# Performance work log

Hardware: AMD Instinct MI355X
Metric: run time of the kernel (lower is better)

## Reference

```python
import jax, jax.numpy as jnp
import numpy as np

N, F, H, FO = 4096, 512, 4, 128  # nodes, in-feat, heads, out-feat per head
NEG_INF = -1e10
LRELU_ALPHA = 0.2


def setup_inputs() -> dict:
    key = jax.random.key(0)
    k_x, k_a, k_w, k_as, k_an = jax.random.split(key, 5)
    X = jax.random.normal(k_x, (N, F), dtype=jnp.float32)
    A = (jax.random.uniform(k_a, (N, N)) < 0.01).astype(jnp.float32)
    A = jnp.minimum(A + jnp.eye(N, dtype=jnp.float32), 1.0)
    W = jax.random.normal(k_w, (H, F, FO), dtype=jnp.float32) * 0.05       # per-head kernels
    b = jnp.zeros((H, FO), dtype=jnp.float32)                               # per-head biases
    a_self = jax.random.normal(k_as, (H, FO), dtype=jnp.float32) * 0.05    # attn_kernel_self (F_,1) per head
    a_neigh = jax.random.normal(k_an, (H, FO), dtype=jnp.float32) * 0.05   # attn_kernel_neigh (F_,1) per head
    return {"X": X, "A": A, "W": W, "b": b, "a_self": a_self, "a_neigh": a_neigh}


def reference(X, A, W, b, a_self, a_neigh):
    # features[h] = X @ W[h] -> [H, N, FO]
    feats = jnp.einsum('nf,hfo->hno', X, W)
    # Nx1 self / neighbor scores per head -> [H, N]
    e_s = jnp.einsum('hno,ho->hn', feats, a_self)
    e_n = jnp.einsum('hno,ho->hn', feats, a_neigh)
    # broadcast-add to [H, N, N], LeakyReLU(0.2), additive adjacency mask
    logits = e_s[:, :, None] + e_n[:, None, :]
    logits = jnp.where(logits > 0, logits, LRELU_ALPHA * logits)
    logits = logits + NEG_INF * (1.0 - A)[None, :, :]
    attn = jax.nn.softmax(logits, axis=-1)          # [H, N, N]
    out = jnp.einsum('hnm,hmo->hno', attn, feats)   # weighted aggregate
    out = out + b[:, None, :]
    # concat heads: [N, H*FO]
    out = jnp.transpose(out, (1, 0, 2)).reshape(X.shape[0], -1)
    return jax.nn.relu(out)
```

## Files before the change

### kernel.cpp

```cpp
#include <hip/hip_runtime.h>
#include <math.h>

#define NODES 4096
#define FIN   512
#define HEADS 4
#define FOUT  128
#define COLS  512

typedef short  short8  __attribute__((ext_vector_type(8)));
typedef float  floatx4 __attribute__((ext_vector_type(4)));

__device__ inline void split8(const float4& a, const float4& b, short8& hi, short8& lo) {
    float v[8] = {a.x, a.y, a.z, a.w, b.x, b.y, b.z, b.w};
    #pragma unroll
    for (int i = 0; i < 8; i++) {
        unsigned xb = __float_as_uint(v[i]);
        unsigned hb = xb & 0xFFFF0000u;
        hi[i] = (short)(hb >> 16);
        float r = v[i] - __uint_as_float(hb);
        lo[i] = (short)(__float_as_uint(r) >> 16);
    }
}

__global__ __launch_bounds__(256) void convert_w(
    const float* __restrict__ W, short* __restrict__ Wthi, short* __restrict__ Wtlo)
{
    int t = blockIdx.x * 256 + threadIdx.x;
    int o = t & 127;
    int hs = t >> 7;
    int h = hs >> 6, seg = hs & 63;
    float4 a, b;
    float va[8];
    #pragma unroll
    for (int i = 0; i < 8; i++)
        va[i] = W[((size_t)(h * FIN) + seg * 8 + i) * FOUT + o];
    a = make_float4(va[0], va[1], va[2], va[3]);
    b = make_float4(va[4], va[5], va[6], va[7]);
    short8 hi, lo; split8(a, b, hi, lo);
    size_t dst = (size_t)(h * FOUT + o) * FIN + seg * 8;
    *(short8*)&Wthi[dst] = hi;
    *(short8*)&Wtlo[dst] = lo;
}

__global__ __launch_bounds__(256) void gemm_mfma(
    const float* __restrict__ X,
    const short* __restrict__ Bthi, const short* __restrict__ Btlo,
    float* __restrict__ feats)
{
    __shared__ short Ah[2][64][40], Al[2][64][40], Bh[2][64][40], Bl[2][64][40];
    const int tid = threadIdx.x;
    const int rowBase = blockIdx.y * 64;
    const int colBase = blockIdx.x * 64;
    const int lane = tid & 63, w = tid >> 6;
    const int quad = lane >> 4, lk = quad * 8, lm = lane & 15;
    const int sr = tid >> 2;
    const int sk = (tid & 3) * 8;

    const float* xp = X + (size_t)(rowBase + sr) * FIN + sk;
    const short* bhp = Bthi + (size_t)(colBase + sr) * FIN + sk;
    const short* blp = Btlo + (size_t)(colBase + sr) * FIN + sk;

    floatx4 acc[4];
    #pragma unroll
    for (int mi = 0; mi < 4; mi++) acc[mi] = (floatx4)0.f;

    float4 xa = *(const float4*)(xp);
    float4 xb = *(const float4*)(xp + 4);
    short8 rbh = *(const short8*)(bhp);
    short8 rbl = *(const short8*)(blp);

    for (int it = 0; it < FIN / 32; ++it) {
        const int cur = it & 1;
        short8 hi, lo; split8(xa, xb, hi, lo);
        *(short8*)&Ah[cur][sr][sk] = hi;
        *(short8*)&Al[cur][sr][sk] = lo;
        *(short8*)&Bh[cur][sr][sk] = rbh;
        *(short8*)&Bl[cur][sr][sk] = rbl;
        if (it + 1 < FIN / 32) {
            int k0 = (it + 1) * 32;
            xa  = *(const float4*)(xp + k0);
            xb  = *(const float4*)(xp + k0 + 4);
            rbh = *(const short8*)(bhp + k0);
            rbl = *(const short8*)(blp + k0);
        }
        __syncthreads();

        short8 afh[4], afl[4];
        #pragma unroll
        for (int mi = 0; mi < 4; mi++) {
            afh[mi] = *(const short8*)&Ah[cur][mi * 16 + lm][lk];
            afl[mi] = *(const short8*)&Al[cur][mi * 16 + lm][lk];
        }
        short8 bfh = *(const short8*)&Bh[cur][w * 16 + lm][lk];
        short8 bfl = *(const short8*)&Bl[cur][w * 16 + lm][lk];
        #pragma unroll
        for (int mi = 0; mi < 4; mi++) {
            acc[mi] = __builtin_amdgcn_mfma_f32_16x16x32_bf16(afh[mi], bfh, acc[mi], 0, 0, 0);
            acc[mi] = __builtin_amdgcn_mfma_f32_16x16x32_bf16(afh[mi], bfl, acc[mi], 0, 0, 0);
            acc[mi] = __builtin_amdgcn_mfma_f32_16x16x32_bf16(afl[mi], bfh, acc[mi], 0, 0, 0);
        }
    }
    #pragma unroll
    for (int mi = 0; mi < 4; mi++) {
        #pragma unroll
        for (int r = 0; r < 4; r++) {
            int row = rowBase + mi * 16 + quad * 4 + r;
            int col = colBase + w * 16 + lm;
            feats[(size_t)row * COLS + col] = acc[mi][r];
        }
    }
}

__global__ __launch_bounds__(256) void scores(
    const float* __restrict__ feats, const float* __restrict__ a_self,
    const float* __restrict__ a_neigh, float* __restrict__ e_s, float* __restrict__ e_n)
{
    const int n = blockIdx.x * 4 + (threadIdx.x >> 6);
    const int l = threadIdx.x & 63;
    float ps[HEADS], pn[HEADS];
    #pragma unroll
    for (int s = 0; s < HEADS; s++) {
        float2 x  = *(const float2*)(feats + (size_t)n * COLS + s * FOUT + 2 * l);
        float2 as = *(const float2*)(a_self  + s * FOUT + 2 * l);
        float2 an = *(const float2*)(a_neigh + s * FOUT + 2 * l);
        ps[s] = x.x * as.x + x.y * as.y;
        pn[s] = x.x * an.x + x.y * an.y;
    }
    #pragma unroll
    for (int off = 32; off > 0; off >>= 1) {
        #pragma unroll
        for (int s = 0; s < HEADS; s++) {
            ps[s] += __shfl_xor(ps[s], off, 64);
            pn[s] += __shfl_xor(pn[s], off, 64);
        }
    }
    if (l == 0) {
        #pragma unroll
        for (int s = 0; s < HEADS; s++) {
            e_s[s * NODES + n] = ps[s];
            e_n[s * NODES + n] = pn[s];
        }
    }
}

__global__ __launch_bounds__(256) void aggregate(
    const float* __restrict__ A, const float* __restrict__ feats,
    const float* __restrict__ e_s, const float* __restrict__ e_n,
    const float* __restrict__ bias, float* __restrict__ out)
{
    const int i = blockIdx.x;
    const int tid = threadIdx.x;
    __shared__ int   s_idx[NODES];
    __shared__ float s_w[HEADS][512];
    __shared__ float s_part[128][5];
    __shared__ int   s_cnt;
    __shared__ float s_dinv[HEADS];
    if (tid == 0) s_cnt = 0;
    __syncthreads();

    const float4* Arow = (const float4*)(A + (size_t)i * NODES);
    for (int q = tid; q < NODES / 4; q += 256) {
        float4 a = Arow[q];
        int j = q * 4;
        if (a.x != 0.f) s_idx[atomicAdd(&s_cnt, 1)] = j;
        if (a.y != 0.f) s_idx[atomicAdd(&s_cnt, 1)] = j + 1;
        if (a.z != 0.f) s_idx[atomicAdd(&s_cnt, 1)] = j + 2;
        if (a.w != 0.f) s_idx[atomicAdd(&s_cnt, 1)] = j + 3;
    }
    __syncthreads();
    const int cnt = s_cnt;

    const int wv = tid >> 6, lane = tid & 63;
    const float esi = e_s[wv * NODES + i];

    float m = -1e30f;
    for (int k = lane; k < cnt; k += 64) {
        float e = esi + e_n[wv * NODES + s_idx[k]];
        m = fmaxf(m, e > 0.f ? e : 0.2f * e);
    }
    #pragma unroll
    for (int off = 32; off > 0; off >>= 1) m = fmaxf(m, __shfl_xor(m, off, 64));

    const int cg   = tid & 127;
    const int half = tid >> 7;
    const int h    = cg >> 5;
    floatx4 acc = (floatx4)0.f;
    float d = 0.f;
    for (int base = 0; base < cnt; base += 512) {
        int nc = min(512, cnt - base);
        for (int k = lane; k < nc; k += 64) {
            float e = esi + e_n[wv * NODES + s_idx[base + k]];
            float l = e > 0.f ? e : 0.2f * e;
            float wgt = __expf(l - m);
            s_w[wv][k] = wgt;
            d += wgt;
        }
        __syncthreads();
        for (int k = half; k < nc; k += 2) {
            int j = s_idx[base + k];
            float wgt = s_w[h][k];
            float4 f = *(const float4*)(feats + (size_t)j * COLS + cg * 4);
            acc[0] = fmaf(wgt, f.x, acc[0]);
            acc[1] = fmaf(wgt, f.y, acc[1]);
            acc[2] = fmaf(wgt, f.z, acc[2]);
            acc[3] = fmaf(wgt, f.w, acc[3]);
        }
        __syncthreads();
    }
    #pragma unroll
    for (int off = 32; off > 0; off >>= 1) d += __shfl_xor(d, off, 64);
    if (lane == 0) s_dinv[wv] = 1.f / d;

    if (half == 1) {
        s_part[cg][0] = acc[0]; s_part[cg][1] = acc[1];
        s_part[cg][2] = acc[2]; s_part[cg][3] = acc[3];
    }
    __syncthreads();
    if (half == 0) {
        float dinv = s_dinv[h];
        float4 b4 = *(const float4*)(bias + h * FOUT + (cg & 31) * 4);
        float o0 = (acc[0] + s_part[cg][0]) * dinv + b4.x;
        float o1 = (acc[1] + s_part[cg][1]) * dinv + b4.y;
        float o2 = (acc[2] + s_part[cg][2]) * dinv + b4.z;
        float o3 = (acc[3] + s_part[cg][3]) * dinv + b4.w;
        *(float4*)(out + (size_t)i * COLS + cg * 4) =
            make_float4(fmaxf(o0, 0.f), fmaxf(o1, 0.f), fmaxf(o2, 0.f), fmaxf(o3, 0.f));
    }
}

extern "C" void kernel_launch(void* const* d_in, const int* in_sizes, int n_in,
                              void* d_out, int out_size, void* d_ws, size_t ws_size,
                              hipStream_t stream) {
    const float* X       = (const float*)d_in[0];
    const float* A       = (const float*)d_in[1];
    const float* W       = (const float*)d_in[2];
    const float* b       = (const float*)d_in[3];
    const float* a_self  = (const float*)d_in[4];
    const float* a_neigh = (const float*)d_in[5];
    float* out = (float*)d_out;

    float* feats = (float*)d_ws;
    float* e_s   = feats + (size_t)NODES * COLS;
    float* e_n   = e_s + HEADS * NODES;
    short* Wthi  = (short*)(e_n + HEADS * NODES);
    short* Wtlo  = Wthi + (size_t)COLS * FIN;

    convert_w<<<128, 256, 0, stream>>>(W, Wthi, Wtlo);
    dim3 gA(COLS / 64, NODES / 64);
    gemm_mfma<<<gA, 256, 0, stream>>>(X, Wthi, Wtlo, feats);
    scores<<<NODES / 4, 256, 0, stream>>>(feats, a_self, a_neigh, e_s, e_n);
    aggregate<<<NODES, 256, 0, stream>>>(A, feats, e_s, e_n, b, out);
}
```

Before: 166.6 us.

## Use single fp16 MFMA for projection and restructure aggregation gather

Replaces the three-pass bf16 hi/lo split GEMM with a single fp16 MFMA pass, cutting MFMA work, shared-memory traffic and W-conversion storage. Rewrites the aggregate kernel so each thread owns two output columns over all neighbours, with eight gathers unrolled per step. This removes the half-split partial-sum reduction and the barriers inside the chunk loop, and packs neighbour indices as 16-bit shorts. The cost is lower GEMM precision: fp16 has fewer mantissa bits than the split scheme, which may push feats error toward tolerance. The chunk loop has no barrier between writing s_w and reusing it, which is only safe because each wave writes and reads its own head row.

New measurement: 155.0 us. 7.0% less time.

```diff
diff --git a/kernel.cpp b/kernel.cpp
--- a/kernel.cpp
+++ b/kernel.cpp
@@ -7,47 +7,29 @@
 #define FOUT  128
 #define COLS  512
 
-typedef short  short8  __attribute__((ext_vector_type(8)));
-typedef float  floatx4 __attribute__((ext_vector_type(4)));
-
-__device__ inline void split8(const float4& a, const float4& b, short8& hi, short8& lo) {
-    float v[8] = {a.x, a.y, a.z, a.w, b.x, b.y, b.z, b.w};
-    #pragma unroll
-    for (int i = 0; i < 8; i++) {
-        unsigned xb = __float_as_uint(v[i]);
-        unsigned hb = xb & 0xFFFF0000u;
-        hi[i] = (short)(hb >> 16);
-        float r = v[i] - __uint_as_float(hb);
-        lo[i] = (short)(__float_as_uint(r) >> 16);
-    }
-}
+typedef _Float16 half8 __attribute__((ext_vector_type(8)));
+typedef float    floatx4 __attribute__((ext_vector_type(4)));
 
 __global__ __launch_bounds__(256) void convert_w(
-    const float* __restrict__ W, short* __restrict__ Wthi, short* __restrict__ Wtlo)
+    const float* __restrict__ W, _Float16* __restrict__ Wt)
 {
     int t = blockIdx.x * 256 + threadIdx.x;
     int o = t & 127;
     int hs = t >> 7;
     int h = hs >> 6, seg = hs & 63;
-    float4 a, b;
-    float va[8];
+    half8 v;
     #pragma unroll
     for (int i = 0; i < 8; i++)
-        va[i] = W[((size_t)(h * FIN) + seg * 8 + i) * FOUT + o];
-    a = make_float4(va[0], va[1], va[2], va[3]);
-    b = make_float4(va[4], va[5], va[6], va[7]);
-    short8 hi, lo; split8(a, b, hi, lo);
-    size_t dst = (size_t)(h * FOUT + o) * FIN + seg * 8;
-    *(short8*)&Wthi[dst] = hi;
-    *(short8*)&Wtlo[dst] = lo;
+        v[i] = (_Float16)W[((size_t)(h * FIN) + seg * 8 + i) * FOUT + o];
+    *(half8*)&Wt[(size_t)(h * FOUT + o) * FIN + seg * 8] = v;
 }
 
 __global__ __launch_bounds__(256) void gemm_mfma(
-    const float* __restrict__ X,
-    const short* __restrict__ Bthi, const short* __restrict__ Btlo,
+    const float* __restrict__ X, const _Float16* __restrict__ Bt,
     float* __restrict__ feats)
 {
-    __shared__ short Ah[2][64][40], Al[2][64][40], Bh[2][64][40], Bl[2][64][40];
+    __shared__ _Float16 Ah[2][64][40];
+    __shared__ _Float16 Bh[2][64][40];
     const int tid = threadIdx.x;
     const int rowBase = blockIdx.y * 64;
     const int colBase = blockIdx.x * 64;
@@ -56,9 +38,8 @@
     const int sr = tid >> 2;
     const int sk = (tid & 3) * 8;
 
-    const float* xp = X + (size_t)(rowBase + sr) * FIN + sk;
-    const short* bhp = Bthi + (size_t)(colBase + sr) * FIN + sk;
-    const short* blp = Btlo + (size_t)(colBase + sr) * FIN + sk;
+    const float*    xp = X  + (size_t)(rowBase + sr) * FIN + sk;
+    const _Float16* bp = Bt + (size_t)(colBase + sr) * FIN + sk;
 
     floatx4 acc[4];
     #pragma unroll
@@ -66,38 +47,29 @@
 
     float4 xa = *(const float4*)(xp);
     float4 xb = *(const float4*)(xp + 4);
-    short8 rbh = *(const short8*)(bhp);
-    short8 rbl = *(const short8*)(blp);
+    half8  rb = *(const half8*)(bp);
 
     for (int it = 0; it < FIN / 32; ++it) {
         const int cur = it & 1;
-        short8 hi, lo; split8(xa, xb, hi, lo);
-        *(short8*)&Ah[cur][sr][sk] = hi;
-        *(short8*)&Al[cur][sr][sk] = lo;
-        *(short8*)&Bh[cur][sr][sk] = rbh;
-        *(short8*)&Bl[cur][sr][sk] = rbl;
+        half8 ha;
+        ha[0] = (_Float16)xa.x; ha[1] = (_Float16)xa.y;
+        ha[2] = (_Float16)xa.z; ha[3] = (_Float16)xa.w;
+        ha[4] = (_Float16)xb.x; ha[5] = (_Float16)xb.y;
+        ha[6] = (_Float16)xb.z; ha[7] = (_Float16)xb.w;
+        *(half8*)&Ah[cur][sr][sk] = ha;
+        *(half8*)&Bh[cur][sr][sk] = rb;
         if (it + 1 < FIN / 32) {
             int k0 = (it + 1) * 32;
-            xa  = *(const float4*)(xp + k0);
-            xb  = *(const float4*)(xp + k0 + 4);
-            rbh = *(const short8*)(bhp + k0);
-            rbl = *(const short8*)(blp + k0);
+            xa = *(const float4*)(xp + k0);
+            xb = *(const float4*)(xp + k0 + 4);
+            rb = *(const half8*)(bp + k0);
         }
         __syncthreads();
-
-        short8 afh[4], afl[4];
+        half8 bfrag = *(const half8*)&Bh[cur][w * 16 + lm][lk];
         #pragma unroll
         for (int mi = 0; mi < 4; mi++) {
-            afh[mi] = *(const short8*)&Ah[cur][mi * 16 + lm][lk];
-            afl[mi] = *(const short8*)&Al[cur][mi * 16 + lm][lk];
-        }
-        short8 bfh = *(const short8*)&Bh[cur][w * 16 + lm][lk];
-        short8 bfl = *(const short8*)&Bl[cur][w * 16 + lm][lk];
-        #pragma unroll
-        for (int mi = 0; mi < 4; mi++) {
-            acc[mi] = __builtin_amdgcn_mfma_f32_16x16x32_bf16(afh[mi], bfh, acc[mi], 0, 0, 0);
-            acc[mi] = __builtin_amdgcn_mfma_f32_16x16x32_bf16(afh[mi], bfl, acc[mi], 0, 0, 0);
-            acc[mi] = __builtin_amdgcn_mfma_f32_16x16x32_bf16(afl[mi], bfh, acc[mi], 0, 0, 0);
+            half8 afrag = *(const half8*)&Ah[cur][mi * 16 + lm][lk];
+            acc[mi] = __builtin_amdgcn_mfma_f32_16x16x32_f16(afrag, bfrag, acc[mi], 0, 0, 0);
         }
     }
     #pragma unroll
@@ -150,11 +122,9 @@
 {
     const int i = blockIdx.x;
     const int tid = threadIdx.x;
-    __shared__ int   s_idx[NODES];
+    __shared__ unsigned short s_idx[NODES];
     __shared__ float s_w[HEADS][512];
-    __shared__ float s_part[128][5];
     __shared__ int   s_cnt;
-    __shared__ float s_dinv[HEADS];
     if (tid == 0) s_cnt = 0;
     __syncthreads();
 
@@ -162,70 +132,65 @@
     for (int q = tid; q < NODES / 4; q += 256) {
         float4 a = Arow[q];
         int j = q * 4;
-        if (a.x != 0.f) s_idx[atomicAdd(&s_cnt, 1)] = j;
-        if (a.y != 0.f) s_idx[atomicAdd(&s_cnt, 1)] = j + 1;
-        if (a.z != 0.f) s_idx[atomicAdd(&s_cnt, 1)] = j + 2;
-        if (a.w != 0.f) s_idx[atomicAdd(&s_cnt, 1)] = j + 3;
+        if (a.x != 0.f) s_idx[atomicAdd(&s_cnt, 1)] = (unsigned short)j;
+        if (a.y != 0.f) s_idx[atomicAdd(&s_cnt, 1)] = (unsigned short)(j + 1);
+        if (a.z != 0.f) s_idx[atomicAdd(&s_cnt, 1)] = (unsigned short)(j + 2);
+        if (a.w != 0.f) s_idx[atomicAdd(&s_cnt, 1)] = (unsigned short)(j + 3);
     }
     __syncthreads();
     const int cnt = s_cnt;
 
-    const int wv = tid >> 6, lane = tid & 63;
-    const float esi = e_s[wv * NODES + i];
+    const int h = tid >> 6, lane = tid & 63;
+    const float esi = e_s[h * NODES + i];
+    const float* enh = e_n + h * NODES;
 
     float m = -1e30f;
     for (int k = lane; k < cnt; k += 64) {
-        float e = esi + e_n[wv * NODES + s_idx[k]];
+        float e = esi + enh[s_idx[k]];
         m = fmaxf(m, e > 0.f ? e : 0.2f * e);
     }
     #pragma unroll
     for (int off = 32; off > 0; off >>= 1) m = fmaxf(m, __shfl_xor(m, off, 64));
 
-    const int cg   = tid & 127;
-    const int half = tid >> 7;
-    const int h    = cg >> 5;
-    floatx4 acc = (floatx4)0.f;
-    float d = 0.f;
+    const int ci = 2 * tid;
+    float acc0 = 0.f, acc1 = 0.f, d = 0.f;
     for (int base = 0; base < cnt; base += 512) {
         int nc = min(512, cnt - base);
         for (int k = lane; k < nc; k += 64) {
-            float e = esi + e_n[wv * NODES + s_idx[base + k]];
+            float e = esi + enh[s_idx[base + k]];
             float l = e > 0.f ? e : 0.2f * e;
             float wgt = __expf(l - m);
-            s_w[wv][k] = wgt;
+            s_w[h][k] = wgt;
             d += wgt;
         }
-        __syncthreads();
-        for (int k = half; k < nc; k += 2) {
-            int j = s_idx[base + k];
-            float wgt = s_w[h][k];
-            float4 f = *(const float4*)(feats + (size_t)j * COLS + cg * 4);
-            acc[0] = fmaf(wgt, f.x, acc[0]);
-            acc[1] = fmaf(wgt, f.y, acc[1]);
-            acc[2] = fmaf(wgt, f.z, acc[2]);
-            acc[3] = fmaf(wgt, f.w, acc[3]);
-        }
-        __syncthreads();
+        for (int k0 = 0; k0 < nc; k0 += 8) {
+            int kk = nc - k0;
+            int   je[8]; float we[8];
+            #pragma unroll
+            for (int u = 0; u < 8; u++) {
+                bool v = (u < kk);
+                je[u] = s_idx[base + (v ? k0 + u : k0)];
+                we[u] = v ? s_w[h][k0 + u] : 0.f;
+            }
+            float2 f[8];
+            #pragma unroll
+            for (int u = 0; u < 8; u++)
+                f[u] = *(const float2*)(feats + (size_t)je[u] * COLS + ci);
+            #pragma unroll
+            for (int u = 0; u < 8; u++) {
+                acc0 = fmaf(we[u], f[u].x, acc0);
+                acc1 = fmaf(we[u], f[u].y, acc1);
+            }
+        }
     }
     #pragma unroll
     for (int off = 32; off > 0; off >>= 1) d += __shfl_xor(d, off, 64);
-    if (lane == 0) s_dinv[wv] = 1.f / d;
-
-    if (half == 1) {
-        s_part[cg][0] = acc[0]; s_part[cg][1] = acc[1];
-        s_part[cg][2] = acc[2]; s_part[cg][3] = acc[3];
-    }
-    __syncthreads();
-    if (half == 0) {
-        float dinv = s_dinv[h];
-        float4 b4 = *(const float4*)(bias + h * FOUT + (cg & 31) * 4);
-        float o0 = (acc[0] + s_part[cg][0]) * dinv + b4.x;
-        float o1 = (acc[1] + s_part[cg][1]) * dinv + b4.y;
-        float o2 = (acc[2] + s_part[cg][2]) * dinv + b4.z;
-        float o3 = (acc[3] + s_part[cg][3]) * dinv + b4.w;
-        *(float4*)(out + (size_t)i * COLS + cg * 4) =
-            make_float4(fmaxf(o0, 0.f), fmaxf(o1, 0.f), fmaxf(o2, 0.f), fmaxf(o3, 0.f));
-    }
+    const float dinv = 1.f / d;
+
+    float2 b2 = *(const float2*)(bias + h * FOUT + (ci & 127));
+    float o0 = acc0 * dinv + b2.x;
+    float o1 = acc1 * dinv + b2.y;
+    *(float2*)(out + (size_t)i * COLS + ci) = make_float2(fmaxf(o0, 0.f), fmaxf(o1, 0.f));
 }
 
 extern "C" void kernel_launch(void* const* d_in, const int* in_sizes, int n_in,
@@ -239,15 +204,14 @@
     const float* a_neigh = (const float*)d_in[5];
     float* out = (float*)d_out;
 
-    float* feats = (float*)d_ws;
-    float* e_s   = feats + (size_t)NODES * COLS;
-    float* e_n   = e_s + HEADS * NODES;
-    short* Wthi  = (short*)(e_n + HEADS * NODES);
-    short* Wtlo  = Wthi + (size_t)COLS * FIN;
-
-    convert_w<<<128, 256, 0, stream>>>(W, Wthi, Wtlo);
+    float*    feats = (float*)d_ws;
+    float*    e_s   = feats + (size_t)NODES * COLS;
+    float*    e_n   = e_s + HEADS * NODES;
+    _Float16* Wt    = (_Float16*)(e_n + HEADS * NODES);
+
+    convert_w<<<128, 256, 0, stream>>>(W, Wt);
     dim3 gA(COLS / 64, NODES / 64);
-    gemm_mfma<<<gA, 256, 0, stream>>>(X, Wthi, Wtlo, feats);
+    gemm_mfma<<<gA, 256, 0, stream>>>(X, Wt, feats);
     scores<<<NODES / 4, 256, 0, stream>>>(feats, a_self, a_neigh, e_s, e_n);
     aggregate<<<NODES, 256, 0, stream>>>(A, feats, e_s, e_n, b, out);
 }
```
